# Kernel optimization log

Hardware: AMD Instinct MI355X
Metric: run time of the kernel (lower is better)

The kernel has to match this reference:

```python
import jax, jax.numpy as jnp
import numpy as np

B, T, C, H, E, MIN_EXPERTS = 4, 2048, 2048, 128, 16, 2
ROPE_BASE = 10000.0


def setup_inputs() -> dict:
    key = jax.random.key(0)
    ks = jax.random.split(key, 6)
    hidden_states = jax.random.normal(ks[0], (B, T, C), jnp.float32)
    position_ids = jnp.arange(T, dtype=jnp.int32)[None, :]  # [1, T]
    sim_matrix = jax.random.normal(ks[1], (C, E), jnp.float32)
    gates = jnp.zeros((E,), jnp.float32)
    s_in = float(np.sqrt(6.0 / (C + H)))   # xavier_uniform bound for (C,H)
    s_out = float(np.sqrt(6.0 / (H + C)))
    q_proj = jax.random.uniform(ks[2], (E, C, H), jnp.float32, -s_in, s_in)
    k_proj = jax.random.uniform(ks[3], (E, C, H), jnp.float32, -s_in, s_in)
    v_proj = jax.random.uniform(ks[4], (E, C, H), jnp.float32, -s_in, s_in)
    o_proj = jax.random.uniform(ks[5], (E, H, C), jnp.float32, -s_out, s_out)
    return dict(hidden_states=hidden_states, position_ids=position_ids,
                sim_matrix=sim_matrix, gates=gates,
                q_proj=q_proj, k_proj=k_proj, v_proj=v_proj, o_proj=o_proj)


def _rotate_half(x):
    h = x.shape[-1] // 2
    return jnp.concatenate([-x[..., h:], x[..., :h]], axis=-1)


def _apply_rope(q, k, position_ids, seq_len, dim, dtype):
    inv_freq = 1.0 / (ROPE_BASE ** (jnp.arange(0, dim, 2, dtype=jnp.float32) / dim))
    t = jnp.arange(seq_len, dtype=jnp.float32)
    freqs = jnp.outer(t, inv_freq)                       # [T, H/2]
    emb = jnp.concatenate([freqs, freqs], axis=-1)       # [T, H]
    cos = jnp.cos(emb).astype(dtype)[position_ids]       # [1, T, H] (broadcasts over batch)
    sin = jnp.sin(emb).astype(dtype)[position_ids]
    q_emb = q * cos + _rotate_half(q) * sin
    k_emb = k * cos + _rotate_half(k) * sin
    return q_emb, k_emb


def reference(hidden_states, position_ids, sim_matrix, gates, q_proj, k_proj, v_proj, o_proj):
    b, t, c = hidden_states.shape
    n = b * t
    h = q_proj.shape[-1]
    x = hidden_states.reshape(n, c)

    # ---- gating: normalize + matmul + sigmoid offset + relu + STE + topk fallback + masked softmax ----
    xn = x / jnp.clip(jnp.linalg.norm(x, axis=-1, keepdims=True), 1e-12)
    wn = sim_matrix / jnp.clip(jnp.linalg.norm(sim_matrix, axis=0, keepdims=True), 1e-12)
    logits = xn @ wn - jax.nn.sigmoid(gates)             # [N, E]
    gated = jax.nn.relu(logits)
    hard = (gated > 0).astype(x.dtype)                   # STE forward (hard 0/1 mask)
    inactive = jnp.sum(hard, axis=1) == 0                # [N]
    _, top_idx = jax.lax.top_k(logits, MIN_EXPERTS)      # [N, MIN]
    fb = jnp.zeros_like(hard).at[jnp.arange(n)[:, None], top_idx].set(1.0)
    mask = jnp.where(inactive[:, None], fb, hard)        # [N, E]
    masked_logits = jnp.where(mask > 0, gated, jnp.asarray(-1e9, gated.dtype))
    routing_weights = jax.nn.softmax(masked_logits, axis=-1)
    # torch only accumulates active (token, expert) pairs -> equivalent to weights * mask
    we = routing_weights * jax.lax.stop_gradient(mask)   # [N, E]

    # ---- per-expert QKV projections, weighted scatter-add (dense-equivalent grouped GEMM) ----
    q = jnp.einsum('ne,nc,ech->nh', we, x, q_proj).reshape(b, t, h)
    k = jnp.einsum('ne,nc,ech->nh', we, x, k_proj).reshape(b, t, h)
    v = jnp.einsum('ne,nc,ech->nh', we, x, v_proj).reshape(b, t, h)

    q, k = _apply_rope(q, k, position_ids, t, h, x.dtype)

    # ---- single-head causal attention ----
    scale = 1.0 / jnp.sqrt(jnp.asarray(h, x.dtype))
    scores = jnp.einsum('bqh,bkh->bqk', q, k) * scale    # [B, T, T]
    causal = jnp.tril(jnp.ones((t, t), bool))
    scores = jnp.where(causal, scores, jnp.finfo(x.dtype).min)
    attn = jnp.einsum('bqk,bkh->bqh', jax.nn.softmax(scores, axis=-1), v)

    # ---- per-expert output projection, weighted scatter-add ----
    attn_flat = attn.reshape(n, h)
    out = jnp.einsum('ne,nh,ehc->nc', we, attn_flat, o_proj).reshape(b, t, c)
    return out
```

## Files before the change

### kernel.cpp

```cpp
#include <hip/hip_runtime.h>
#include <hip/hip_fp16.h>

#define T_ 2048
#define C_ 2048
#define H_ 128
#define E_ 16
#define N_TOK 8192
#define SCALE_ 0.08838834764831845f

typedef _Float16 f16;
typedef _Float16 f16x4 __attribute__((ext_vector_type(4)));
typedef _Float16 f16x8 __attribute__((ext_vector_type(8)));
typedef float f32x4 __attribute__((ext_vector_type(4)));
typedef unsigned int u32x4 __attribute__((ext_vector_type(4)));

#define MFMA(a,b,c) __builtin_amdgcn_mfma_f32_16x16x32_f16(a,b,c,0,0,0)

__device__ __forceinline__ void gload16(const void* g, void* l){
  __builtin_amdgcn_global_load_lds(
      (const __attribute__((address_space(1))) unsigned int*)g,
      (__attribute__((address_space(3))) unsigned int*)l, 16, 0, 0);
}

__global__ __launch_bounds__(256) void prep_kernel(const float* __restrict__ sim,
    const float* __restrict__ gates, double* __restrict__ wninv, double* __restrict__ sigg){
  __shared__ double part[16][17];
  int tid = threadIdx.x;
  int col = tid & 15, grp = tid >> 4;
  double ssq = 0.0;
  for (int r = grp; r < C_; r += 16){ float v = sim[r*E_ + col]; ssq += (double)v*(double)v; }
  part[grp][col] = ssq;
  __syncthreads();
  if (tid < E_){
    double s = 0.0;
    #pragma unroll
    for (int g2 = 0; g2 < 16; g2++) s += part[g2][tid];
    wninv[tid] = 1.0 / fmax(sqrt(s), 1e-12);
    sigg[tid]  = 1.0 / (1.0 + exp(-(double)gates[tid]));
  }
}

__global__ __launch_bounds__(256) void conv_x(const float* __restrict__ x, f16* __restrict__ xh){
  for (int v = blockIdx.x*256 + threadIdx.x; v < N_TOK*C_/4; v += 4096*256){
    f32x4 a = *(const f32x4*)&x[(size_t)v*4];
    f16x4 h; h[0]=(f16)a[0]; h[1]=(f16)a[1]; h[2]=(f16)a[2]; h[3]=(f16)a[3];
    *(f16x4*)&xh[(size_t)v*4] = h;
  }
}

__global__ __launch_bounds__(256) void conv_w(const float* __restrict__ qp,
    const float* __restrict__ kp, const float* __restrict__ vp, f16* __restrict__ wT){
  int ep = blockIdx.z; int e = ep/3, proj = ep - 3*e;
  const float* W = (proj==0?qp:(proj==1?kp:vp)) + (size_t)e*C_*H_;
  int k0 = blockIdx.x*64, j0 = blockIdx.y*64;
  __shared__ float t[64][65];
  int tid = threadIdx.x;
  #pragma unroll
  for (int i = 0; i < 4; i++){
    int s = tid + 256*i;
    int r = s >> 4, c4 = (s & 15)*4;
    f32x4 a = *(const f32x4*)&W[(size_t)(k0+r)*H_ + j0 + c4];
    t[r][c4]=a[0]; t[r][c4+1]=a[1]; t[r][c4+2]=a[2]; t[r][c4+3]=a[3];
  }
  __syncthreads();
  #pragma unroll
  for (int i = 0; i < 4; i++){
    int s = tid + 256*i;
    int jj = s >> 4, k4 = (s & 15)*4;
    f16x4 h;
    h[0]=(f16)t[k4][jj]; h[1]=(f16)t[k4+1][jj]; h[2]=(f16)t[k4+2][jj]; h[3]=(f16)t[k4+3][jj];
    *(f16x4*)&wT[((size_t)e*384 + proj*128 + j0 + jj)*C_ + k0 + k4] = h;
  }
}

__global__ __launch_bounds__(256) void conv_o(const float* __restrict__ op, f16* __restrict__ oT){
  int e = blockIdx.z;
  int n0 = blockIdx.x*64, k0 = blockIdx.y*64;
  __shared__ float t[64][65];
  int tid = threadIdx.x;
  #pragma unroll
  for (int i = 0; i < 4; i++){
    int s = tid + 256*i;
    int r = s >> 4, c4 = (s & 15)*4;
    f32x4 a = *(const f32x4*)&op[(size_t)e*H_*C_ + (size_t)(k0+r)*C_ + n0 + c4];
    t[r][c4]=a[0]; t[r][c4+1]=a[1]; t[r][c4+2]=a[2]; t[r][c4+3]=a[3];
  }
  __syncthreads();
  #pragma unroll
  for (int i = 0; i < 4; i++){
    int s = tid + 256*i;
    int nn = s >> 4, k4 = (s & 15)*4;
    f16x4 h;
    h[0]=(f16)t[k4][nn]; h[1]=(f16)t[k4+1][nn]; h[2]=(f16)t[k4+2][nn]; h[3]=(f16)t[k4+3][nn];
    *(f16x4*)&oT[((size_t)e*C_ + n0 + nn)*H_ + k0 + k4] = h;
  }
}

__global__ __launch_bounds__(256) void gate_kernel(const float* __restrict__ x,
    const float* __restrict__ sim, const double* __restrict__ wninv,
    const double* __restrict__ sigg, int* __restrict__ cnt,
    int* __restrict__ list, float* __restrict__ listw){
  __shared__ __align__(16) float st[4096];
  __shared__ double dred[32][17];
  int tid = threadIdx.x;
  int eq = tid >> 6, l = tid & 63;
  int tok = l & 31, kh = l >> 5;
  int n0 = blockIdx.x * 32;
  const float* xr = x + (size_t)(n0 + tok) * C_;
  double accA[4] = {0,0,0,0}, accB[4] = {0,0,0,0};
  double ssqA = 0.0, ssqB = 0.0;
  for (int k0 = 0; k0 < C_; k0 += 256){
    __syncthreads();
    #pragma unroll
    for (int i = 0; i < 4; i++){
      int idx = tid + 256*i;
      *(f32x4*)&st[idx*4] = *(const f32x4*)&sim[(size_t)k0*E_ + idx*4];
    }
    __syncthreads();
    #pragma unroll
    for (int q = 0; q < 32; q++){
      int kl = kh*128 + q*4;
      f32x4 xv = *(const f32x4*)&xr[k0 + kl];
      #pragma unroll
      for (int j = 0; j < 4; j++){
        f32x4 sv = *(const f32x4*)&st[(kl+j)*E_ + eq*4];
        double xd = (double)xv[j];
        if (j & 1){
          accB[0] += xd*(double)sv[0]; accB[1] += xd*(double)sv[1];
          accB[2] += xd*(double)sv[2]; accB[3] += xd*(double)sv[3];
          if (eq == 0) ssqB += xd*xd;
        } else {
          accA[0] += xd*(double)sv[0]; accA[1] += xd*(double)sv[1];
          accA[2] += xd*(double)sv[2]; accA[3] += xd*(double)sv[3];
          if (eq == 0) ssqA += xd*xd;
        }
      }
    }
  }
  double acc[4];
  #pragma unroll
  for (int j = 0; j < 4; j++){
    acc[j] = accA[j] + accB[j];
    acc[j] += __shfl_xor(acc[j], 32);
  }
  double ssq = ssqA + ssqB;
  ssq += __shfl_xor(ssq, 32);
  if (l < 32){
    #pragma unroll
    for (int j = 0; j < 4; j++) dred[tok][eq*4 + j] = acc[j];
    if (eq == 0) dred[tok][16] = ssq;
  }
  __syncthreads();
  if (tid < 32){
    int n = n0 + tid;
    double inv = 1.0 / fmax(sqrt(dred[tid][16]), 1e-12);
    double logit[E_]; bool mask[E_]; int active = 0;
    #pragma unroll
    for (int e = 0; e < E_; e++){
      logit[e] = dred[tid][e] * inv * wninv[e] - sigg[e];
      mask[e] = logit[e] > 0.0;
      if (mask[e]) active++;
    }
    if (active == 0){
      int i1 = -1, i2 = -1; double b1 = -1e300, b2 = -1e300;
      for (int e = 0; e < E_; e++){
        double v = logit[e];
        if (v > b1){ b2 = b1; i2 = i1; b1 = v; i1 = e; }
        else if (v > b2){ b2 = v; i2 = e; }
      }
      mask[i1] = true; mask[i2] = true;
    }
    double mx = -1e300;
    for (int e = 0; e < E_; e++){ if (mask[e]) mx = fmax(mx, fmax(logit[e], 0.0)); }
    double ex[E_]; double sum = 0.0;
    for (int e = 0; e < E_; e++){
      double gval = fmax(logit[e], 0.0);
      ex[e] = mask[e] ? exp(gval - mx) : 0.0;
      sum += ex[e];
    }
    double isum = 1.0 / sum;
    for (int e = 0; e < E_; e++){
      if (mask[e]){
        int p = atomicAdd(&cnt[e], 1);
        list[e*N_TOK + p]  = n;
        listw[e*N_TOK + p] = (float)(ex[e]*isum);
      }
    }
  }
}

__global__ __launch_bounds__(64) void tile_builder(const int* __restrict__ cnt,
    int* __restrict__ tlist, int* __restrict__ ntile,
    int* __restrict__ tlist2, int* __restrict__ ntile2){
  __shared__ int nts[E_], nts2[E_];
  int tid = threadIdx.x;
  if (tid < E_){
    nts[tid]  = (cnt[tid] + 63) >> 6;
    nts2[tid] = (cnt[tid] + 127) >> 7;
  }
  __syncthreads();
  if (tid < E_){
    int base = 0, b2 = 0;
    for (int e = 0; e < tid; e++){ base += nts[e]; b2 += nts2[e]; }
    for (int t = 0; t < nts[tid];  t++) tlist[base + t] = (tid << 8) | t;
    for (int t = 0; t < nts2[tid]; t++) tlist2[b2 + t]  = (tid << 8) | t;
    if (tid == E_-1){ *ntile = base + nts[tid]; *ntile2 = b2 + nts2[tid]; }
  }
}

__global__ __launch_bounds__(256, 2) void qkv_gemm(const f16* __restrict__ xh,
    const f16* __restrict__ wT, const int* __restrict__ cnt,
    const int* __restrict__ list, const float* __restrict__ listw,
    const int* __restrict__ tlist2, const int* __restrict__ ntile2,
    float* __restrict__ qkv){
  __shared__ __align__(16) f16 a_s[2][128][64];
  __shared__ __align__(16) f16 b_s[2][128][64];
  __shared__ int tok_s[128];
  __shared__ float wgt_s[128];
  int nitems = (*ntile2) * 3;
  int tid = threadIdx.x;
  int l = tid & 63, wv = tid >> 6;
  int wm = wv >> 1, wn = wv & 1;
  int g = l >> 4, c = l & 15;
  for (int w = blockIdx.x; w < nitems; w += gridDim.x){
    int tile = w / 3, nb = w - tile*3;
    int ent = tlist2[tile];
    int e = ent >> 8, mt = ent & 255;
    int ce = cnt[e];
    int m0 = mt * 128;
    if (tid < 128){
      int gr = m0 + tid;
      tok_s[tid] = (gr < ce) ? list[e*N_TOK + gr] : 0;
      wgt_s[tid] = (gr < ce) ? listw[e*N_TOK + gr] : 0.f;
    }
    __syncthreads();
    const f16* Bbase = wT + ((size_t)e*384 + nb*128)*C_;
    const f16* agp[4]; const f16* bgp[4];
    #pragma unroll
    for (int i = 0; i < 4; i++){
      int id = tid + 256*i;
      int row = id >> 3, ch = id & 7;
      agp[i] = xh + (size_t)tok_s[row]*C_ + ch*8;
      bgp[i] = Bbase + (size_t)row*C_ + ch*8;
    }
    f32x4 acc[4][4];
    #pragma unroll
    for (int m = 0; m < 4; m++)
      #pragma unroll
      for (int n = 0; n < 4; n++) acc[m][n] = (f32x4){0.f,0.f,0.f,0.f};
    #pragma unroll
    for (int i = 0; i < 4; i++){
      int id = tid + 256*i;
      gload16(agp[i], &a_s[0][0][0] + (size_t)id*8);
      gload16(bgp[i], &b_s[0][0][0] + (size_t)id*8);
    }
    __syncthreads();
    int cur = 0;
    for (int k0 = 0; k0 < C_; k0 += 64){
      int nxt = k0 + 64;
      if (nxt < C_){
        int nb2 = cur ^ 1;
        #pragma unroll
        for (int i = 0; i < 4; i++){
          int id = tid + 256*i;
          gload16(agp[i] + nxt, &a_s[nb2][0][0] + (size_t)id*8);
          gload16(bgp[i] + nxt, &b_s[nb2][0][0] + (size_t)id*8);
        }
      }
      #pragma unroll
      for (int ks = 0; ks < 2; ks++){
        f16x8 af[4], bf[4];
        #pragma unroll
        for (int m = 0; m < 4; m++)
          af[m] = *(const f16x8*)&a_s[cur][wm*64 + m*16 + c][ks*32 + 8*g];
        #pragma unroll
        for (int n = 0; n < 4; n++)
          bf[n] = *(const f16x8*)&b_s[cur][wn*64 + n*16 + c][ks*32 + 8*g];
        #pragma unroll
        for (int m = 0; m < 4; m++)
          #pragma unroll
          for (int n = 0; n < 4; n++)
            acc[m][n] = MFMA(af[m], bf[n], acc[m][n]);
      }
      __syncthreads();
      cur ^= 1;
    }
    #pragma unroll
    for (int m = 0; m < 4; m++){
      #pragma unroll
      for (int i = 0; i < 4; i++){
        int row = wm*64 + m*16 + 4*g + i;
        int gr = m0 + row;
        if (gr < ce){
          int tok = tok_s[row]; float wgt = wgt_s[row];
          #pragma unroll
          for (int n = 0; n < 4; n++){
            int col = nb*128 + wn*64 + n*16 + c;
            atomicAdd(&qkv[(size_t)tok*384 + col], wgt*acc[m][n][i]);
          }
        }
      }
    }
    __syncthreads();
  }
}

__global__ __launch_bounds__(192) void rope_kernel(const float* __restrict__ qkv,
    const int* __restrict__ pos_ids, f16* __restrict__ qh, f16* __restrict__ kh,
    f16* __restrict__ vh){
  int n = blockIdx.x; int tid = threadIdx.x;
  const float* row = qkv + (size_t)n * 384;
  if (tid < 128){
    int isK = tid >> 6, j = tid & 63;
    const float* src = row + isK*H_;
    float a = src[j], b = src[j+64];
    int pos = pos_ids[n & (T_-1)];
    float freq = exp2f(-(float)j * 0.20762050593046015f);
    float ang = (float)pos * freq;
    float s, cc;
    sincosf(ang, &s, &cc);
    f16* dst = isK ? kh : qh;
    dst[(size_t)n*H_ + j]      = (f16)(a*cc - b*s);
    dst[(size_t)n*H_ + j + 64] = (f16)(b*cc + a*s);
  } else {
    int j = (tid - 128)*2;
    vh[(size_t)n*H_ + j]     = (f16)row[256 + j];
    vh[(size_t)n*H_ + j + 1] = (f16)row[256 + j + 1];
  }
}

#define LDK_ 136
#define LDV_ 72
__global__ __launch_bounds__(128) void attn_kernel(const f16* __restrict__ qh,
    const f16* __restrict__ kh, const f16* __restrict__ vh, f16* __restrict__ ah){
  int bid = blockIdx.x;
  int b = bid >> 6, qt = bid & 63;
  int q0 = qt*32, nbase = b*T_;
  __shared__ __align__(16) f16 q_s[32*LDK_];
  __shared__ __align__(16) f16 k_s[64*LDK_];
  __shared__ __align__(16) f16 v_s[128*LDV_];
  __shared__ __align__(16) f16 p_s[2*16*LDV_];
  int tid = threadIdx.x;
  int l = tid & 63, w = tid >> 6;
  int g = l >> 4, c = l & 15;
  #pragma unroll
  for (int i = 0; i < 4; i++){
    int slot = tid + 128*i;
    int ch = slot & 15, r = slot >> 4;
    *(u32x4*)&q_s[r*LDK_ + ch*8] = *(const u32x4*)&qh[((size_t)(nbase + q0 + r))*H_ + ch*8];
  }
  f32x4 oacc[8];
  #pragma unroll
  for (int nb = 0; nb < 8; nb++) oacc[nb] = (f32x4){0,0,0,0};
  float m_run[4], l_run[4];
  #pragma unroll
  for (int i = 0; i < 4; i++){ m_run[i] = -1e30f; l_run[i] = 0.f; }
  int nk = (q0 + 31)/64 + 1;
  for (int kt = 0; kt < nk; kt++){
    int kb = kt*64;
    __syncthreads();
    #pragma unroll
    for (int i = 0; i < 8; i++){
      int slot = tid + 128*i;
      int ch = slot & 15, r = slot >> 4;
      *(u32x4*)&k_s[r*LDK_ + ch*8] = *(const u32x4*)&kh[((size_t)(nbase + kb + r))*H_ + ch*8];
    }
    #pragma unroll
    for (int i = 0; i < 8; i++){
      int slot = tid + 128*i;
      int tok = slot & 63, ch = slot >> 6;
      f16x8 raw = *(const f16x8*)&vh[((size_t)(nbase + kb + tok))*H_ + ch*8];
      #pragma unroll
      for (int j = 0; j < 8; j++) v_s[(ch*8 + j)*LDV_ + tok] = raw[j];
    }
    __syncthreads();
    f32x4 sacc[4];
    #pragma unroll
    for (int f = 0; f < 4; f++) sacc[f] = (f32x4){0,0,0,0};
    #pragma unroll
    for (int ks = 0; ks < 4; ks++){
      f16x8 qf = *(const f16x8*)&q_s[(w*16 + c)*LDK_ + ks*32 + 8*g];
      #pragma unroll
      for (int f = 0; f < 4; f++){
        f16x8 kf = *(const f16x8*)&k_s[(f*16 + c)*LDK_ + ks*32 + 8*g];
        sacc[f] = MFMA(qf, kf, sacc[f]);
      }
    }
    float tm[4];
    #pragma unroll
    for (int i = 0; i < 4; i++) tm[i] = -1e30f;
    #pragma unroll
    for (int f = 0; f < 4; f++){
      int kg = kb + f*16 + c;
      #pragma unroll
      for (int i = 0; i < 4; i++){
        int qg = q0 + w*16 + 4*g + i;
        float s = sacc[f][i] * SCALE_;
        if (kg > qg) s = -1e30f;
        sacc[f][i] = s;
        tm[i] = fmaxf(tm[i], s);
      }
    }
    #pragma unroll
    for (int i = 0; i < 4; i++){
      #pragma unroll
      for (int d = 1; d <= 8; d <<= 1) tm[i] = fmaxf(tm[i], __shfl_xor(tm[i], d));
      float mn = fmaxf(m_run[i], tm[i]);
      float al = __expf(m_run[i] - mn);
      m_run[i] = mn;
      l_run[i] *= al;
      #pragma unroll
      for (int nb = 0; nb < 8; nb++) oacc[nb][i] *= al;
    }
    float rs[4] = {0.f,0.f,0.f,0.f};
    #pragma unroll
    for (int f = 0; f < 4; f++){
      #pragma unroll
      for (int i = 0; i < 4; i++){
        float p = __expf(sacc[f][i] - m_run[i]);
        rs[i] += p;
        p_s[w*16*LDV_ + (4*g + i)*LDV_ + f*16 + c] = (f16)p;
      }
    }
    #pragma unroll
    for (int i = 0; i < 4; i++){
      #pragma unroll
      for (int d = 1; d <= 8; d <<= 1) rs[i] += __shfl_xor(rs[i], d);
      l_run[i] += rs[i];
    }
    #pragma unroll
    for (int ks = 0; ks < 2; ks++){
      f16x8 pf = *(const f16x8*)&p_s[w*16*LDV_ + c*LDV_ + ks*32 + 8*g];
      #pragma unroll
      for (int nb = 0; nb < 8; nb++){
        f16x8 vf = *(const f16x8*)&v_s[(c + 16*nb)*LDV_ + ks*32 + 8*g];
        oacc[nb] = MFMA(pf, vf, oacc[nb]);
      }
    }
  }
  #pragma unroll
  for (int i = 0; i < 4; i++){
    float inv = 1.f / l_run[i];
    int qg = q0 + w*16 + 4*g + i;
    #pragma unroll
    for (int nb = 0; nb < 8; nb++)
      ah[((size_t)(nbase + qg))*H_ + c + 16*nb] = (f16)(oacc[nb][i] * inv);
  }
}

#define LDT 136
__global__ __launch_bounds__(256) void o_gemm(const f16* __restrict__ ah,
    const f16* __restrict__ oT, const int* __restrict__ cnt,
    const int* __restrict__ list, const float* __restrict__ listw,
    const int* __restrict__ tlist, const int* __restrict__ ntile,
    float* __restrict__ out){
  __shared__ __align__(16) f16 a_s[64*LDT];
  __shared__ __align__(16) f16 b_s[128*LDT];
  __shared__ int tok_s[64];
  __shared__ float wgt_s[64];
  int nitems = (*ntile) * 16;
  int tid = threadIdx.x;
  int l = tid & 63, wv = tid >> 6;
  int wm = wv >> 1, wn = wv & 1;
  int g = l >> 4, c = l & 15;
  for (int w = blockIdx.x; w < nitems; w += gridDim.x){
    int tile = w >> 4, nbt = w & 15;
    int ent = tlist[tile];
    int e = ent >> 8, mt = ent & 255;
    int ce = cnt[e];
    int m0 = mt * 64, n0 = nbt * 128;
    if (tid < 64){
      int gr = m0 + tid;
      tok_s[tid] = (gr < ce) ? list[e*N_TOK + gr] : 0;
      wgt_s[tid] = (gr < ce) ? listw[e*N_TOK + gr] : 0.f;
    }
    __syncthreads();
    #pragma unroll
    for (int i = 0; i < 4; i++){
      int s = tid + 256*i;
      int r = s >> 4, cs = (s & 15)*8;
      f16x8 v = *(const f16x8*)&ah[(size_t)tok_s[r]*H_ + cs];
      float wgt = wgt_s[r];
      f16x8 o;
      #pragma unroll
      for (int j = 0; j < 8; j++) o[j] = (f16)((float)v[j]*wgt);
      *(f16x8*)&a_s[r*LDT + cs] = o;
    }
    #pragma unroll
    for (int i = 0; i < 8; i++){
      int s = tid + 256*i;
      int j = s >> 4, cs = (s & 15)*8;
      f16x8 v = *(const f16x8*)&oT[((size_t)e*C_ + n0 + j)*H_ + cs];
      *(f16x8*)&b_s[j*LDT + cs] = v;
    }
    __syncthreads();
    f32x4 acc[2][4];
    #pragma unroll
    for (int m = 0; m < 2; m++)
      #pragma unroll
      for (int n = 0; n < 4; n++) acc[m][n] = (f32x4){0.f,0.f,0.f,0.f};
    #pragma unroll
    for (int ks = 0; ks < 4; ks++){
      f16x8 af[2], bf[4];
      #pragma unroll
      for (int m = 0; m < 2; m++)
        af[m] = *(const f16x8*)&a_s[(wm*32 + m*16 + c)*LDT + ks*32 + 8*g];
      #pragma unroll
      for (int n = 0; n < 4; n++)
        bf[n] = *(const f16x8*)&b_s[(wn*64 + n*16 + c)*LDT + ks*32 + 8*g];
      #pragma unroll
      for (int m = 0; m < 2; m++)
        #pragma unroll
        for (int n = 0; n < 4; n++)
          acc[m][n] = MFMA(af[m], bf[n], acc[m][n]);
    }
    #pragma unroll
    for (int m = 0; m < 2; m++){
      #pragma unroll
      for (int i = 0; i < 4; i++){
        int row = wm*32 + m*16 + 4*g + i;
        int gr = m0 + row;
        if (gr < ce){
          int tok = tok_s[row];
          #pragma unroll
          for (int n = 0; n < 4; n++){
            int col = n0 + wn*64 + n*16 + c;
            atomicAdd(&out[(size_t)tok*C_ + col], acc[m][n][i]);
          }
        }
      }
    }
    __syncthreads();
  }
}

extern "C" void kernel_launch(void* const* d_in, const int* in_sizes, int n_in,
                              void* d_out, int out_size, void* d_ws, size_t ws_size,
                              hipStream_t stream){
  const float* hs    = (const float*)d_in[0];
  const int*   pos   = (const int*)d_in[1];
  const float* sim   = (const float*)d_in[2];
  const float* gates = (const float*)d_in[3];
  const float* qp    = (const float*)d_in[4];
  const float* kp    = (const float*)d_in[5];
  const float* vp    = (const float*)d_in[6];
  const float* op    = (const float*)d_in[7];
  float* out = (float*)d_out;
  char* ws = (char*)d_ws;
  int*    cnt    = (int*)(ws + 0);
  int*    ntile  = (int*)(ws + 64);
  double* wninv  = (double*)(ws + 128);
  double* sigg   = (double*)(ws + 256);
  int*    tlist  = (int*)(ws + 512);
  int*    list   = (int*)(ws + 8704);
  float*  listw  = (float*)(ws + 532992);
  f16*    xh     = (f16*)(ws + 1057280);
  f16*    wT     = (f16*)(ws + 34611712);
  f16*    oT     = (f16*)(ws + 59777536);
  float*  qkv    = (float*)(ws + 68166144);
  f16*    ah     = (f16*)(ws + 68166144);
  f16*    qh     = (f16*)(ws + 80749056);
  f16*    kh     = (f16*)(ws + 82846208);
  f16*    vh     = (f16*)(ws + 84943360);
  int*    tlist2 = (int*)(ws + 87040512);
  int*    ntile2 = (int*)(ws + 87044608);

  hipMemsetAsync(cnt, 0, 64, stream);
  hipMemsetAsync(qkv, 0, (size_t)N_TOK*384*4, stream);
  hipMemsetAsync(out, 0, (size_t)N_TOK*C_*4, stream);

  prep_kernel<<<1, 256, 0, stream>>>(sim, gates, wninv, sigg);
  conv_x<<<4096, 256, 0, stream>>>(hs, xh);
  conv_w<<<dim3(32, 2, 48), 256, 0, stream>>>(qp, kp, vp, wT);
  conv_o<<<dim3(32, 2, 16), 256, 0, stream>>>(op, oT);
  gate_kernel<<<256, 256, 0, stream>>>(hs, sim, wninv, sigg, cnt, list, listw);
  tile_builder<<<1, 64, 0, stream>>>(cnt, tlist, ntile, tlist2, ntile2);
  qkv_gemm<<<512, 256, 0, stream>>>(xh, wT, cnt, list, listw, tlist2, ntile2, qkv);
  rope_kernel<<<N_TOK, 192, 0, stream>>>(qkv, pos, qh, kh, vh);
  attn_kernel<<<256, 128, 0, stream>>>(qh, kh, vh, ah);
  o_gemm<<<2048, 256, 0, stream>>>(ah, oT, cnt, list, listw, tlist, ntile, out);
}
```

Before: 622.0 us.

## Split attention KV range across blocks with merge pass; regrid gate kernel

The attention kernel now splits each query tile's key range into four interleaved segments across a second grid dimension. It writes unnormalized partial outputs and running max/sum to a workspace, and a new merge kernel combines them into the final f16 output. Separately, the gating kernel processes 8 tokens per block over 1024 blocks and reads the similarity matrix directly from global memory instead of staging it in LDS. Both changes aim to raise parallelism on an under-occupied GPU, at the cost of extra fp32 partial-result traffic, an extra launch, and reuse of the xh buffer region for the partials.

```diff
diff --git a/kernel.cpp b/kernel.cpp
--- a/kernel.cpp
+++ b/kernel.cpp
@@ -6,6 +6,7 @@
 #define H_ 128
 #define E_ 16
 #define N_TOK 8192
+#define NS_ 4
 #define SCALE_ 0.08838834764831845f
 
 typedef _Float16 f16;
@@ -100,40 +101,31 @@
     const float* __restrict__ sim, const double* __restrict__ wninv,
     const double* __restrict__ sigg, int* __restrict__ cnt,
     int* __restrict__ list, float* __restrict__ listw){
-  __shared__ __align__(16) float st[4096];
-  __shared__ double dred[32][17];
-  int tid = threadIdx.x;
-  int eq = tid >> 6, l = tid & 63;
-  int tok = l & 31, kh = l >> 5;
-  int n0 = blockIdx.x * 32;
+  __shared__ double dred[8][17];
+  int tid = threadIdx.x;
+  int wv = tid >> 6, l = tid & 63;
+  int tok = l & 7, ko = l >> 3;
+  int n0 = blockIdx.x * 8;
   const float* xr = x + (size_t)(n0 + tok) * C_;
+  const float* sp = sim + wv*4;
   double accA[4] = {0,0,0,0}, accB[4] = {0,0,0,0};
   double ssqA = 0.0, ssqB = 0.0;
-  for (int k0 = 0; k0 < C_; k0 += 256){
-    __syncthreads();
-    #pragma unroll
-    for (int i = 0; i < 4; i++){
-      int idx = tid + 256*i;
-      *(f32x4*)&st[idx*4] = *(const f32x4*)&sim[(size_t)k0*E_ + idx*4];
-    }
-    __syncthreads();
-    #pragma unroll
-    for (int q = 0; q < 32; q++){
-      int kl = kh*128 + q*4;
-      f32x4 xv = *(const f32x4*)&xr[k0 + kl];
-      #pragma unroll
-      for (int j = 0; j < 4; j++){
-        f32x4 sv = *(const f32x4*)&st[(kl+j)*E_ + eq*4];
-        double xd = (double)xv[j];
-        if (j & 1){
-          accB[0] += xd*(double)sv[0]; accB[1] += xd*(double)sv[1];
-          accB[2] += xd*(double)sv[2]; accB[3] += xd*(double)sv[3];
-          if (eq == 0) ssqB += xd*xd;
-        } else {
-          accA[0] += xd*(double)sv[0]; accA[1] += xd*(double)sv[1];
-          accA[2] += xd*(double)sv[2]; accA[3] += xd*(double)sv[3];
-          if (eq == 0) ssqA += xd*xd;
-        }
+  int kbase = ko * 256;
+  #pragma unroll 4
+  for (int k = kbase; k < kbase + 256; k += 4){
+    f32x4 xv = *(const f32x4*)&xr[k];
+    #pragma unroll
+    for (int j = 0; j < 4; j++){
+      f32x4 sv = *(const f32x4*)&sp[(size_t)(k+j)*E_];
+      double xd = (double)xv[j];
+      if (j & 1){
+        accB[0] += xd*(double)sv[0]; accB[1] += xd*(double)sv[1];
+        accB[2] += xd*(double)sv[2]; accB[3] += xd*(double)sv[3];
+        if (wv == 0) ssqB += xd*xd;
+      } else {
+        accA[0] += xd*(double)sv[0]; accA[1] += xd*(double)sv[1];
+        accA[2] += xd*(double)sv[2]; accA[3] += xd*(double)sv[3];
+        if (wv == 0) ssqA += xd*xd;
       }
     }
   }
@@ -141,17 +133,21 @@
   #pragma unroll
   for (int j = 0; j < 4; j++){
     acc[j] = accA[j] + accB[j];
+    acc[j] += __shfl_xor(acc[j], 8);
+    acc[j] += __shfl_xor(acc[j], 16);
     acc[j] += __shfl_xor(acc[j], 32);
   }
   double ssq = ssqA + ssqB;
+  ssq += __shfl_xor(ssq, 8);
+  ssq += __shfl_xor(ssq, 16);
   ssq += __shfl_xor(ssq, 32);
-  if (l < 32){
-    #pragma unroll
-    for (int j = 0; j < 4; j++) dred[tok][eq*4 + j] = acc[j];
-    if (eq == 0) dred[tok][16] = ssq;
+  if (l < 8){
+    #pragma unroll
+    for (int j = 0; j < 4; j++) dred[tok][wv*4 + j] = acc[j];
+    if (wv == 0) dred[tok][16] = ssq;
   }
   __syncthreads();
-  if (tid < 32){
+  if (tid < 8){
     int n = n0 + tid;
     double inv = 1.0 / fmax(sqrt(dred[tid][16]), 1e-12);
     double logit[E_]; bool mask[E_]; int active = 0;
@@ -332,8 +328,10 @@
 #define LDK_ 136
 #define LDV_ 72
 __global__ __launch_bounds__(128) void attn_kernel(const f16* __restrict__ qh,
-    const f16* __restrict__ kh, const f16* __restrict__ vh, f16* __restrict__ ah){
+    const f16* __restrict__ kh, const f16* __restrict__ vh,
+    float* __restrict__ Opart, float* __restrict__ mlpart){
   int bid = blockIdx.x;
+  int seg = blockIdx.y;
   int b = bid >> 6, qt = bid & 63;
   int q0 = qt*32, nbase = b*T_;
   __shared__ __align__(16) f16 q_s[32*LDK_];
@@ -356,7 +354,7 @@
   #pragma unroll
   for (int i = 0; i < 4; i++){ m_run[i] = -1e30f; l_run[i] = 0.f; }
   int nk = (q0 + 31)/64 + 1;
-  for (int kt = 0; kt < nk; kt++){
+  for (int kt = seg; kt < nk; kt += NS_){
     int kb = kt*64;
     __syncthreads();
     #pragma unroll
@@ -440,11 +438,49 @@
   }
   #pragma unroll
   for (int i = 0; i < 4; i++){
-    float inv = 1.f / l_run[i];
-    int qg = q0 + w*16 + 4*g + i;
+    int row = w*16 + 4*g + i;
+    size_t base = ((size_t)(seg*256 + bid)*32 + row);
+    if (c == 0){
+      mlpart[base*2]     = m_run[i];
+      mlpart[base*2 + 1] = l_run[i];
+    }
+    float* orow = Opart + base*128;
     #pragma unroll
     for (int nb = 0; nb < 8; nb++)
-      ah[((size_t)(nbase + qg))*H_ + c + 16*nb] = (f16)(oacc[nb][i] * inv);
+      orow[c + 16*nb] = oacc[nb][i];
+  }
+}
+
+__global__ __launch_bounds__(128) void attn_merge(const float* __restrict__ Opart,
+    const float* __restrict__ mlpart, f16* __restrict__ ah){
+  int bid = blockIdx.x;
+  int tid = threadIdx.x;
+  int row = tid & 31, d0 = (tid >> 5) * 32;
+  float ms[NS_], lv[NS_], wgt[NS_];
+  float m = -3e38f;
+  #pragma unroll
+  for (int s = 0; s < NS_; s++){
+    size_t base = ((size_t)(s*256 + bid)*32 + row);
+    ms[s] = mlpart[base*2];
+    lv[s] = mlpart[base*2 + 1];
+    m = fmaxf(m, ms[s]);
+  }
+  float wsum = 0.f;
+  #pragma unroll
+  for (int s = 0; s < NS_; s++){ wgt[s] = __expf(ms[s] - m); wsum += wgt[s]*lv[s]; }
+  float inv = 1.f / wsum;
+  int token = (bid >> 6)*T_ + (bid & 63)*32 + row;
+  #pragma unroll
+  for (int dd = 0; dd < 32; dd += 4){
+    f32x4 o = (f32x4){0,0,0,0};
+    #pragma unroll
+    for (int s = 0; s < NS_; s++){
+      f32x4 p = *(const f32x4*)&Opart[(((size_t)(s*256 + bid)*32 + row))*128 + d0 + dd];
+      o[0] += wgt[s]*p[0]; o[1] += wgt[s]*p[1]; o[2] += wgt[s]*p[2]; o[3] += wgt[s]*p[3];
+    }
+    f16x4 h;
+    h[0]=(f16)(o[0]*inv); h[1]=(f16)(o[1]*inv); h[2]=(f16)(o[2]*inv); h[3]=(f16)(o[3]*inv);
+    *(f16x4*)&ah[(size_t)token*H_ + d0 + dd] = h;
   }
 }
 
@@ -555,6 +591,8 @@
   int*    list   = (int*)(ws + 8704);
   float*  listw  = (float*)(ws + 532992);
   f16*    xh     = (f16*)(ws + 1057280);
+  float*  Opart  = (float*)(ws + 1057280);
+  float*  mlpart = (float*)(ws + 17834496);
   f16*    wT     = (f16*)(ws + 34611712);
   f16*    oT     = (f16*)(ws + 59777536);
   float*  qkv    = (float*)(ws + 68166144);
@@ -573,10 +611,11 @@
   conv_x<<<4096, 256, 0, stream>>>(hs, xh);
   conv_w<<<dim3(32, 2, 48), 256, 0, stream>>>(qp, kp, vp, wT);
   conv_o<<<dim3(32, 2, 16), 256, 0, stream>>>(op, oT);
-  gate_kernel<<<256, 256, 0, stream>>>(hs, sim, wninv, sigg, cnt, list, listw);
+  gate_kernel<<<1024, 256, 0, stream>>>(hs, sim, wninv, sigg, cnt, list, listw);
   tile_builder<<<1, 64, 0, stream>>>(cnt, tlist, ntile, tlist2, ntile2);
   qkv_gemm<<<512, 256, 0, stream>>>(xh, wT, cnt, list, listw, tlist2, ntile2, qkv);
   rope_kernel<<<N_TOK, 192, 0, stream>>>(qkv, pos, qh, kh, vh);
-  attn_kernel<<<256, 128, 0, stream>>>(qh, kh, vh, ah);
+  attn_kernel<<<dim3(256, NS_), 128, 0, stream>>>(qh, kh, vh, Opart, mlpart);
+  attn_merge<<<256, 128, 0, stream>>>(Opart, mlpart, ah);
   o_gemm<<<2048, 256, 0, stream>>>(ah, oT, cnt, list, listw, tlist, ntile, out);
 }
```

Result: slower. 674.3 us (+8.4%).
